# Optimization experiments

Hardware: AMD Instinct MI355X
Metric: run time of the kernel (lower is better)

Reference implementation:

```python
import jax, jax.numpy as jnp
import numpy as np

# pywt db4 decomposition filters (8 taps)
DEC_LO = np.array([-0.010597401784997278, 0.032883011666982945, 0.030841381835986965,
                   -0.18703481171888114, -0.02798376941698385, 0.6308807679295904,
                   0.7148465705525415, 0.23037781330885523], dtype=np.float32)
DEC_HI = np.array([-0.23037781330885523, 0.7148465705525415, -0.6308807679295904,
                   -0.02798376941698385, 0.18703481171888114, 0.030841381835986965,
                   -0.032883011666982945, -0.010597401784997278], dtype=np.float32)
LEVEL = 6
F = 8  # filter length

# pywt dwt with mode='zero' is exactly full_convolve(x, filt)[1::2].
# We realize it as a strided correlation with the flipped filters:
# out[i] = sum_j x_pad[2i+j] * filt[F-1-j], x padded left by F-2 zeros.
_KERNEL = jnp.asarray(np.stack([DEC_LO[::-1], DEC_HI[::-1]])[:, None, :])  # [2,1,F]

def _dwt_step(x):
    # x: [B, N] -> (cA [B, M], cD [B, M]) with M = floor((N+F-1)/2)
    N = x.shape[-1]
    M = (N + F - 1) // 2
    xp = jnp.pad(x, ((0, 0), (F - 2, F)))[:, None, :]          # [B,1,Npad]
    y = jax.lax.conv_general_dilated(
        xp, _KERNEL.astype(x.dtype), window_strides=(2,), padding='VALID',
        dimension_numbers=('NCH', 'OIH', 'NCH'))                # [B,2,>=M]
    return y[:, 0, :M], y[:, 1, :M]


def setup_inputs() -> dict:
    key = jax.random.key(0)
    x = jax.random.normal(key, (64, 262144), dtype=jnp.float32)
    return {"x": x}


def reference(x):
    # Cascaded 6-level db4 DWT, zero boundary mode.
    a = x
    details = []  # finest first
    for _ in range(LEVEL):
        a, d = _dwt_step(a)
        details.append(d)
    # Match torch module: details[0] = coarsest detail (pywt coeffs[1])
    return (a,) + tuple(details[::-1])
```

## Files before the change

kernel.cpp:

```cpp
#include <hip/hip_runtime.h>


#define NTHREADS 256
#define TT 64
#define LEN0 (64*TT + 378)
#define LEN1 (32*TT + 186)
#define LEN2 (16*TT + 90)
#define LEN3 (8*TT + 42)
#define LEN4 (4*TT + 18)
#define LEN5 (2*TT + 6)
#define LEN6 (TT)

#define N0 262144
#define M1 131075
#define M2 65541
#define M3 32774
#define M4 16390
#define M5 8198
#define M6 4102

#define OFF_A6 ((size_t)0)
#define OFF_D6 ((size_t)262528)
#define OFF_D5 ((size_t)525056)
#define OFF_D4 ((size_t)1049728)
#define OFF_D3 ((size_t)2098688)
#define OFF_D2 ((size_t)4196224)
#define OFF_D1 ((size_t)8390848)

__device__ __constant__ float c_lo[8] = {
    -0.010597401784997278f, 0.032883011666982945f, 0.030841381835986965f,
    -0.18703481171888114f, -0.02798376941698385f, 0.6308807679295904f,
    0.7148465705525415f, 0.23037781330885523f};
__device__ __constant__ float c_hi[8] = {
    -0.23037781330885523f, 0.7148465705525415f, -0.6308807679295904f,
    -0.02798376941698385f, 0.18703481171888114f, 0.030841381835986965f,
    -0.032883011666982945f, -0.010597401784997278f};

__device__ inline void dwt_step_lds(const float* __restrict__ s,
                                    float* __restrict__ d,
                                    int base, int len, int M, int cOff,
                                    float* __restrict__ dglob, int tid) {
  for (int l = tid; l < len; l += NTHREADS) {
    int g = base + l;
    float a = 0.f, dt = 0.f;
    if (g >= 0 && g < M) {
#pragma unroll
      for (int t = 0; t < 8; ++t) {
        float v = s[2 * l + 7 - t];
        a = fmaf(c_lo[t], v, a);
        dt = fmaf(c_hi[t], v, dt);
      }
    }
    d[l] = a;
    if (l >= cOff && g < M) dglob[g] = dt;
  }
}

__global__ __launch_bounds__(NTHREADS) void dwt6_kernel(
    const float* __restrict__ x, float* __restrict__ out) {
  const int p = blockIdx.x;
  const int row = blockIdx.y;
  const int tid = threadIdx.x;

  __shared__ float bufA[LEN0];
  __shared__ float bufB[LEN1];

  const int b6 = p * TT;
  const int b5 = 2 * b6 - 6;
  const int b4 = 2 * b5 - 6;
  const int b3 = 2 * b4 - 6;
  const int b2 = 2 * b3 - 6;
  const int b1 = 2 * b2 - 6;
  const int b0 = 2 * b1 - 6;

  const float* __restrict__ xr = x + (size_t)row * N0;
  for (int l = tid; l < LEN0; l += NTHREADS) {
    int g = b0 + l;
    bufA[l] = (g >= 0 && g < N0) ? xr[g] : 0.0f;
  }
  __syncthreads();

  dwt_step_lds(bufA, bufB, b1, LEN1, M1, 186, out + OFF_D1 + (size_t)row * M1, tid);
  __syncthreads();
  dwt_step_lds(bufB, bufA, b2, LEN2, M2, 90, out + OFF_D2 + (size_t)row * M2, tid);
  __syncthreads();
  dwt_step_lds(bufA, bufB, b3, LEN3, M3, 42, out + OFF_D3 + (size_t)row * M3, tid);
  __syncthreads();
  dwt_step_lds(bufB, bufA, b4, LEN4, M4, 18, out + OFF_D4 + (size_t)row * M4, tid);
  __syncthreads();
  dwt_step_lds(bufA, bufB, b5, LEN5, M5, 6, out + OFF_D5 + (size_t)row * M5, tid);
  __syncthreads();

  for (int l = tid; l < LEN6; l += NTHREADS) {
    int g = b6 + l;
    if (g < M6) {
      float a = 0.f, dt = 0.f;
#pragma unroll
      for (int t = 0; t < 8; ++t) {
        float v = bufB[2 * l + 7 - t];
        a = fmaf(c_lo[t], v, a);
        dt = fmaf(c_hi[t], v, dt);
      }
      out[OFF_A6 + (size_t)row * M6 + g] = a;
      out[OFF_D6 + (size_t)row * M6 + g] = dt;
    }
  }
}

extern "C" void kernel_launch(void* const* d_in, const int* in_sizes, int n_in,
                              void* d_out, int out_size, void* d_ws, size_t ws_size,
                              hipStream_t stream) {
  const float* x = (const float*)d_in[0];
  float* out = (float*)d_out;
  dim3 grid(65, 64);
  dwt6_kernel<<<grid, NTHREADS, 0, stream>>>(x, out);
}
```

Baseline: 137.2 us.

## Add bounds-free vectorized fast path for interior tiles of cascaded DWT

Interior tiles (blocks 1..63) now skip all boundary checks: the input is loaded with float2 global reads, and each level computes four outputs per thread from float4 LDS reads held in registers. Detail coefficients are stored without per-element range tests. Edge tiles keep the original scalar path with reversed filter constants, and a launch-bounds occupancy hint is added. The aim is to cut LDS instruction count and branch overhead, at the cost of more registers and duplicated code.

```diff
diff --git a/kernel.cpp b/kernel.cpp
--- a/kernel.cpp
+++ b/kernel.cpp
@@ -1,15 +1,14 @@
 #include <hip/hip_runtime.h>
 
 
-#define NTHREADS 256
+#define NT 256
 #define TT 64
-#define LEN0 (64*TT + 378)
-#define LEN1 (32*TT + 186)
-#define LEN2 (16*TT + 90)
-#define LEN3 (8*TT + 42)
-#define LEN4 (4*TT + 18)
-#define LEN5 (2*TT + 6)
-#define LEN6 (TT)
+#define LEN0 4474
+#define LEN1 2234
+#define LEN2 1114
+#define LEN3 554
+#define LEN4 274
+#define LEN5 134
 
 #define N0 262144
 #define M1 131075
@@ -27,28 +26,64 @@
 #define OFF_D2 ((size_t)4196224)
 #define OFF_D1 ((size_t)8390848)
 
-__device__ __constant__ float c_lo[8] = {
-    -0.010597401784997278f, 0.032883011666982945f, 0.030841381835986965f,
-    -0.18703481171888114f, -0.02798376941698385f, 0.6308807679295904f,
-    0.7148465705525415f, 0.23037781330885523f};
-__device__ __constant__ float c_hi[8] = {
-    -0.23037781330885523f, 0.7148465705525415f, -0.6308807679295904f,
-    -0.02798376941698385f, 0.18703481171888114f, 0.030841381835986965f,
-    -0.032883011666982945f, -0.010597401784997278f};
+__device__ __constant__ float RLO[8] = {
+    0.23037781330885523f, 0.7148465705525415f, 0.6308807679295904f,
+    -0.02798376941698385f, -0.18703481171888114f, 0.030841381835986965f,
+    0.032883011666982945f, -0.010597401784997278f};
+__device__ __constant__ float RHI[8] = {
+    -0.010597401784997278f, -0.032883011666982945f, 0.030841381835986965f,
+    0.18703481171888114f, -0.02798376941698385f, -0.6308807679295904f,
+    0.7148465705525415f, -0.23037781330885523f};
 
-__device__ inline void dwt_step_lds(const float* __restrict__ s,
-                                    float* __restrict__ d,
-                                    int base, int len, int M, int cOff,
-                                    float* __restrict__ dglob, int tid) {
-  for (int l = tid; l < len; l += NTHREADS) {
+template <int LEN, int NC>
+__device__ __forceinline__ void level_fast(const float4* __restrict__ s4,
+                                           float4* __restrict__ d4,
+                                           float* __restrict__ dg) {
+  for (int c = threadIdx.x; c < NC; c += NT) {
+    float4 q0 = s4[2 * c + 0];
+    float4 q1 = s4[2 * c + 1];
+    float4 q2 = s4[2 * c + 2];
+    float4 q3 = s4[2 * c + 3];
+    float w[16] = {q0.x, q0.y, q0.z, q0.w, q1.x, q1.y, q1.z, q1.w,
+                   q2.x, q2.y, q2.z, q2.w, q3.x, q3.y, q3.z, q3.w};
+    float a[4], d[4];
+#pragma unroll
+    for (int j = 0; j < 4; ++j) {
+      float aa = 0.f, dd = 0.f;
+#pragma unroll
+      for (int m = 0; m < 8; ++m) {
+        aa = fmaf(RLO[m], w[2 * j + m], aa);
+        dd = fmaf(RHI[m], w[2 * j + m], dd);
+      }
+      a[j] = aa;
+      d[j] = dd;
+    }
+    d4[c] = make_float4(a[0], a[1], a[2], a[3]);
+    const int l0 = 4 * c;
+    if (l0 + 4 <= LEN) {
+#pragma unroll
+      for (int j = 0; j < 4; ++j) dg[l0 + j] = d[j];
+    } else {
+#pragma unroll
+      for (int j = 0; j < 4; ++j)
+        if (l0 + j < LEN) dg[l0 + j] = d[j];
+    }
+  }
+}
+
+__device__ inline void dwt_step_slow(const float* __restrict__ s,
+                                     float* __restrict__ d, int base, int len,
+                                     int M, int cOff, float* __restrict__ dglob,
+                                     int tid) {
+  for (int l = tid; l < len; l += NT) {
     int g = base + l;
     float a = 0.f, dt = 0.f;
     if (g >= 0 && g < M) {
 #pragma unroll
-      for (int t = 0; t < 8; ++t) {
-        float v = s[2 * l + 7 - t];
-        a = fmaf(c_lo[t], v, a);
-        dt = fmaf(c_hi[t], v, dt);
+      for (int m = 0; m < 8; ++m) {
+        float v = s[2 * l + m];
+        a = fmaf(RLO[m], v, a);
+        dt = fmaf(RHI[m], v, dt);
       }
     }
     d[l] = a;
@@ -56,14 +91,16 @@
   }
 }
 
-__global__ __launch_bounds__(NTHREADS) void dwt6_kernel(
-    const float* __restrict__ x, float* __restrict__ out) {
+__global__ __launch_bounds__(NT, 5) void dwt6_kernel(const float* __restrict__ x,
+                                                     float* __restrict__ out) {
   const int p = blockIdx.x;
   const int row = blockIdx.y;
   const int tid = threadIdx.x;
 
-  __shared__ float bufA[LEN0];
-  __shared__ float bufB[LEN1];
+  __shared__ float4 bufA4[1120];
+  __shared__ float4 bufB4[560];
+  float* bufA = (float*)bufA4;
+  float* bufB = (float*)bufB4;
 
   const int b6 = p * TT;
   const int b5 = 2 * b6 - 6;
@@ -73,45 +110,89 @@
   const int b1 = 2 * b2 - 6;
   const int b0 = 2 * b1 - 6;
 
-  const float* __restrict__ xr = x + (size_t)row * N0;
-  for (int l = tid; l < LEN0; l += NTHREADS) {
-    int g = b0 + l;
-    bufA[l] = (g >= 0 && g < N0) ? xr[g] : 0.0f;
-  }
-  __syncthreads();
+  const size_t r1 = (size_t)row * M1, r2 = (size_t)row * M2,
+               r3 = (size_t)row * M3, r4 = (size_t)row * M4,
+               r5 = (size_t)row * M5, r6 = (size_t)row * M6;
 
-  dwt_step_lds(bufA, bufB, b1, LEN1, M1, 186, out + OFF_D1 + (size_t)row * M1, tid);
-  __syncthreads();
-  dwt_step_lds(bufB, bufA, b2, LEN2, M2, 90, out + OFF_D2 + (size_t)row * M2, tid);
-  __syncthreads();
-  dwt_step_lds(bufA, bufB, b3, LEN3, M3, 42, out + OFF_D3 + (size_t)row * M3, tid);
-  __syncthreads();
-  dwt_step_lds(bufB, bufA, b4, LEN4, M4, 18, out + OFF_D4 + (size_t)row * M4, tid);
-  __syncthreads();
-  dwt_step_lds(bufA, bufB, b5, LEN5, M5, 6, out + OFF_D5 + (size_t)row * M5, tid);
-  __syncthreads();
+  if (p >= 1 && p <= 63) {
+    const float2* __restrict__ xs = (const float2*)(x + (size_t)row * N0 + b0);
+    float2* __restrict__ bA2 = (float2*)bufA;
+    for (int m = tid; m < LEN0 / 2; m += NT) bA2[m] = xs[m];
+    __syncthreads();
 
-  for (int l = tid; l < LEN6; l += NTHREADS) {
-    int g = b6 + l;
-    if (g < M6) {
-      float a = 0.f, dt = 0.f;
+    level_fast<LEN1, 559>(bufA4, bufB4, out + OFF_D1 + r1 + b1);
+    __syncthreads();
+    level_fast<LEN2, 279>(bufB4, bufA4, out + OFF_D2 + r2 + b2);
+    __syncthreads();
+    level_fast<LEN3, 139>(bufA4, bufB4, out + OFF_D3 + r3 + b3);
+    __syncthreads();
+    level_fast<LEN4, 69>(bufB4, bufA4, out + OFF_D4 + r4 + b4);
+    __syncthreads();
+    level_fast<LEN5, 34>(bufA4, bufB4, out + OFF_D5 + r5 + b5);
+    __syncthreads();
+
+    float* __restrict__ ga = out + OFF_A6 + r6 + b6;
+    float* __restrict__ gd = out + OFF_D6 + r6 + b6;
+    for (int c = tid; c < 16; c += NT) {
+      float4 q0 = bufB4[2 * c + 0];
+      float4 q1 = bufB4[2 * c + 1];
+      float4 q2 = bufB4[2 * c + 2];
+      float4 q3 = bufB4[2 * c + 3];
+      float w[16] = {q0.x, q0.y, q0.z, q0.w, q1.x, q1.y, q1.z, q1.w,
+                     q2.x, q2.y, q2.z, q2.w, q3.x, q3.y, q3.z, q3.w};
 #pragma unroll
-      for (int t = 0; t < 8; ++t) {
-        float v = bufB[2 * l + 7 - t];
-        a = fmaf(c_lo[t], v, a);
-        dt = fmaf(c_hi[t], v, dt);
+      for (int j = 0; j < 4; ++j) {
+        float aa = 0.f, dd = 0.f;
+#pragma unroll
+        for (int m = 0; m < 8; ++m) {
+          aa = fmaf(RLO[m], w[2 * j + m], aa);
+          dd = fmaf(RHI[m], w[2 * j + m], dd);
+        }
+        ga[4 * c + j] = aa;
+        gd[4 * c + j] = dd;
       }
-      out[OFF_A6 + (size_t)row * M6 + g] = a;
-      out[OFF_D6 + (size_t)row * M6 + g] = dt;
+    }
+  } else {
+    const float* __restrict__ xr = x + (size_t)row * N0;
+    for (int l = tid; l < LEN0; l += NT) {
+      int g = b0 + l;
+      bufA[l] = (g >= 0 && g < N0) ? xr[g] : 0.0f;
+    }
+    __syncthreads();
+
+    dwt_step_slow(bufA, bufB, b1, LEN1, M1, 186, out + OFF_D1 + r1, tid);
+    __syncthreads();
+    dwt_step_slow(bufB, bufA, b2, LEN2, M2, 90, out + OFF_D2 + r2, tid);
+    __syncthreads();
+    dwt_step_slow(bufA, bufB, b3, LEN3, M3, 42, out + OFF_D3 + r3, tid);
+    __syncthreads();
+    dwt_step_slow(bufB, bufA, b4, LEN4, M4, 18, out + OFF_D4 + r4, tid);
+    __syncthreads();
+    dwt_step_slow(bufA, bufB, b5, LEN5, M5, 6, out + OFF_D5 + r5, tid);
+    __syncthreads();
+
+    for (int l = tid; l < TT; l += NT) {
+      int g = b6 + l;
+      if (g < M6) {
+        float a = 0.f, dt = 0.f;
+#pragma unroll
+        for (int m = 0; m < 8; ++m) {
+          float v = bufB[2 * l + m];
+          a = fmaf(RLO[m], v, a);
+          dt = fmaf(RHI[m], v, dt);
+        }
+        out[OFF_A6 + r6 + g] = a;
+        out[OFF_D6 + r6 + g] = dt;
+      }
     }
   }
 }
 
 extern "C" void kernel_launch(void* const* d_in, const int* in_sizes, int n_in,
-                              void* d_out, int out_size, void* d_ws, size_t ws_size,
-                              hipStream_t stream) {
+                              void* d_out, int out_size, void* d_ws,
+                              size_t ws_size, hipStream_t stream) {
   const float* x = (const float*)d_in[0];
   float* out = (float*)d_out;
   dim3 grid(65, 64);
-  dwt6_kernel<<<grid, NTHREADS, 0, stream>>>(x, out);
+  dwt6_kernel<<<grid, NT, 0, stream>>>(x, out);
 }
```

Result: faster. 123.7 us (-9.8%).
